# Optimization experiments

Measured on AMD Instinct MI355X. Metric: run time of the kernel, lower is better.

The kernel has to match this reference:

```python
import jax, jax.numpy as jnp
import numpy as np

N_NODES = 100000
N_EDGES = 800000
F_IN = 64
UNITS = 64


def setup_inputs() -> dict:
    key = jax.random.key(0)
    k1, k2, k3, k4, k5, k6 = jax.random.split(key, 6)
    x = jax.random.normal(k1, (N_NODES, F_IN), dtype=jnp.float32)
    w = jax.random.normal(k2, (F_IN, UNITS), dtype=jnp.float32)
    b = jax.random.normal(k3, (UNITS,), dtype=jnp.float32)
    edge_weight = jax.random.uniform(k4, (N_EDGES,), dtype=jnp.float32)
    edge_row = jax.random.randint(k5, (N_EDGES,), 0, N_NODES, dtype=jnp.int32)
    edge_col = jax.random.randint(k6, (N_EDGES,), 0, N_NODES, dtype=jnp.int32)
    return {"x": x, "w": w, "b": b, "edge_weight": edge_weight,
            "edge_row": edge_row, "edge_col": edge_col}


def reference(x, w, b, edge_weight, edge_row, edge_col):
    # GCN layer: out = A_hat @ (X W) + b, A_hat given in COO form.
    xw = jnp.matmul(x, w)                          # [N, units] dense projection
    msgs = xw[edge_col] * edge_weight[:, None]     # [E, units] gather + scale
    out = jax.ops.segment_sum(msgs, edge_row, num_segments=N_NODES)  # SpMM reduce
    return out + b
```

## Files before the change

### kernel.cpp

```cpp
#include <hip/hip_runtime.h>
#include <hip/hip_fp16.h>

#define N_NODES 100000
#define N_EDGES 800000
#define FDIM 64
#define TILE_ROWS 32
#define N_TILES (N_NODES / TILE_ROWS)
#define SCAN_BLOCK 1024
#define N_SCAN_BLOCKS ((N_NODES + SCAN_BLOCK - 1) / SCAN_BLOCK)

__global__ __launch_bounds__(256) void gemm_hist_kernel(
    const float* __restrict__ x, const float* __restrict__ w,
    const int* __restrict__ erow, __half* __restrict__ xwh,
    int* __restrict__ count) {
    const int tid = threadIdx.x;
    const int bid = blockIdx.x;

    const int e = bid * 256 + tid;
    if (e < N_EDGES) atomicAdd(&count[erow[e]], 1);

    __shared__ float wq[16 * 64 * 4];
    __shared__ float xs[TILE_ROWS * FDIM];

    const int lane = tid & 63;
    const int wid = tid >> 6;

    float4* wq4 = reinterpret_cast<float4*>(wq);
    #pragma unroll
    for (int it = 0; it < 4; ++it) {
        const int k0 = wid * 4 + it;
        float4 wv;
        wv.x = w[(4 * k0 + 0) * FDIM + lane];
        wv.y = w[(4 * k0 + 1) * FDIM + lane];
        wv.z = w[(4 * k0 + 2) * FDIM + lane];
        wv.w = w[(4 * k0 + 3) * FDIM + lane];
        wq4[k0 * 64 + lane] = wv;
    }

    {
        const float4* xg4 = reinterpret_cast<const float4*>(
            x + (size_t)bid * TILE_ROWS * FDIM);
        float4* xs4 = reinterpret_cast<float4*>(xs);
        xs4[tid] = xg4[tid];
        xs4[256 + tid] = xg4[256 + tid];
    }
    __syncthreads();

    const float4* xs4 = reinterpret_cast<const float4*>(xs);
    const int rbase = wid * 8;
    float acc[8] = {0.f, 0.f, 0.f, 0.f, 0.f, 0.f, 0.f, 0.f};
    #pragma unroll 4
    for (int k0 = 0; k0 < 16; ++k0) {
        const float4 wv = wq4[k0 * 64 + lane];
        #pragma unroll
        for (int rr = 0; rr < 8; ++rr) {
            const float4 xv = xs4[(rbase + rr) * 16 + k0];
            acc[rr] += xv.x * wv.x + xv.y * wv.y + xv.z * wv.z + xv.w * wv.w;
        }
    }

    const int growbase = bid * TILE_ROWS + rbase;
    #pragma unroll
    for (int rr = 0; rr < 8; ++rr)
        xwh[(size_t)(growbase + rr) * FDIM + lane] = __float2half(acc[rr]);
}

__global__ __launch_bounds__(SCAN_BLOCK) void scan_block_kernel(
    const int* __restrict__ count, int* __restrict__ starts,
    int* __restrict__ blockSums) {
    __shared__ int tmp[SCAN_BLOCK];
    const int tid = threadIdx.x;
    const int i = blockIdx.x * SCAN_BLOCK + tid;
    const int v = (i < N_NODES) ? count[i] : 0;
    tmp[tid] = v;
    __syncthreads();
    for (int off = 1; off < SCAN_BLOCK; off <<= 1) {
        int t = (tid >= off) ? tmp[tid - off] : 0;
        __syncthreads();
        tmp[tid] += t;
        __syncthreads();
    }
    if (i < N_NODES) starts[i] = tmp[tid] - v;
    if (tid == SCAN_BLOCK - 1) blockSums[blockIdx.x] = tmp[tid];
}

__global__ __launch_bounds__(256) void scanadd_kernel(
    int* __restrict__ starts, const int* __restrict__ blockSums,
    int* __restrict__ cursor) {
    __shared__ int ssum[128];
    const int tid = threadIdx.x;
    if (tid < 128) ssum[tid] = (tid < N_SCAN_BLOCKS) ? blockSums[tid] : 0;
    __syncthreads();
    for (int off = 1; off < 128; off <<= 1) {
        int t = (tid < 128 && tid >= off) ? ssum[tid - off] : 0;
        __syncthreads();
        if (tid < 128) ssum[tid] += t;
        __syncthreads();
    }
    const int i = blockIdx.x * 256 + tid;
    if (i < N_NODES) {
        const int j = i >> 10;
        const int add = (j == 0) ? 0 : ssum[j - 1];
        const int s = starts[i] + add;
        starts[i] = s;
        cursor[i] = s;
    } else if (i == N_NODES) {
        starts[N_NODES] = N_EDGES;
    }
}

__global__ __launch_bounds__(256) void fill_kernel(
    const int* __restrict__ erow, const int* __restrict__ ecol,
    const float* __restrict__ ew, int* __restrict__ cursor,
    uint2* __restrict__ recs) {
    const int base = (blockIdx.x * 256 + threadIdx.x) * 4;
    if (base + 3 < N_EDGES) {
        int4 r = *reinterpret_cast<const int4*>(erow + base);
        int4 c = *reinterpret_cast<const int4*>(ecol + base);
        float4 wt = *reinterpret_cast<const float4*>(ew + base);
        int p0 = atomicAdd(&cursor[r.x], 1);
        int p1 = atomicAdd(&cursor[r.y], 1);
        int p2 = atomicAdd(&cursor[r.z], 1);
        int p3 = atomicAdd(&cursor[r.w], 1);
        recs[p0] = make_uint2((unsigned)c.x, __float_as_uint(wt.x));
        recs[p1] = make_uint2((unsigned)c.y, __float_as_uint(wt.y));
        recs[p2] = make_uint2((unsigned)c.z, __float_as_uint(wt.z));
        recs[p3] = make_uint2((unsigned)c.w, __float_as_uint(wt.w));
    } else {
        for (int e = base; e < N_EDGES; ++e) {
            int p = atomicAdd(&cursor[erow[e]], 1);
            recs[p] = make_uint2((unsigned)ecol[e], __float_as_uint(ew[e]));
        }
    }
}

__global__ __launch_bounds__(256) void aggregate_h_kernel(
    const __half* __restrict__ xwh, const uint2* __restrict__ recs,
    const int* __restrict__ starts, const float* __restrict__ b,
    float* __restrict__ out) {
    const int lane = threadIdx.x & 63;
    const int g = lane >> 4;
    const int s = lane & 15;
    const int wave = (int)((blockIdx.x * blockDim.x + threadIdx.x) >> 6);
    const int nwaves = (int)((gridDim.x * (size_t)blockDim.x) >> 6);
    const float4 bias = reinterpret_cast<const float4*>(b)[s];
    const unsigned long long* recs8 =
        reinterpret_cast<const unsigned long long*>(recs);

    for (int r0 = wave * 4; r0 < N_NODES; r0 += nwaves * 4) {
        const int r = r0 + g;
        if (r < N_NODES) {
            const int st = starts[r];
            const int cnt = starts[r + 1] - st;
            float4 acc = bias;
            int k = 0;
            for (; k + 4 <= cnt; k += 4) {
                unsigned long long p0 = __builtin_nontemporal_load(recs8 + st + k + 0);
                unsigned long long p1 = __builtin_nontemporal_load(recs8 + st + k + 1);
                unsigned long long p2 = __builtin_nontemporal_load(recs8 + st + k + 2);
                unsigned long long p3 = __builtin_nontemporal_load(recs8 + st + k + 3);
                uint2 g0 = *reinterpret_cast<const uint2*>(
                    xwh + (size_t)(unsigned)p0 * FDIM + 4 * s);
                uint2 g1 = *reinterpret_cast<const uint2*>(
                    xwh + (size_t)(unsigned)p1 * FDIM + 4 * s);
                uint2 g2 = *reinterpret_cast<const uint2*>(
                    xwh + (size_t)(unsigned)p2 * FDIM + 4 * s);
                uint2 g3 = *reinterpret_cast<const uint2*>(
                    xwh + (size_t)(unsigned)p3 * FDIM + 4 * s);
                const float w0 = __uint_as_float((unsigned)(p0 >> 32));
                const float w1 = __uint_as_float((unsigned)(p1 >> 32));
                const float w2 = __uint_as_float((unsigned)(p2 >> 32));
                const float w3 = __uint_as_float((unsigned)(p3 >> 32));
                float2 a0 = __half22float2(*reinterpret_cast<__half2*>(&g0.x));
                float2 b0 = __half22float2(*reinterpret_cast<__half2*>(&g0.y));
                float2 a1 = __half22float2(*reinterpret_cast<__half2*>(&g1.x));
                float2 b1 = __half22float2(*reinterpret_cast<__half2*>(&g1.y));
                float2 a2 = __half22float2(*reinterpret_cast<__half2*>(&g2.x));
                float2 b2 = __half22float2(*reinterpret_cast<__half2*>(&g2.y));
                float2 a3 = __half22float2(*reinterpret_cast<__half2*>(&g3.x));
                float2 b3 = __half22float2(*reinterpret_cast<__half2*>(&g3.y));
                acc.x += a0.x * w0 + a1.x * w1 + a2.x * w2 + a3.x * w3;
                acc.y += a0.y * w0 + a1.y * w1 + a2.y * w2 + a3.y * w3;
                acc.z += b0.x * w0 + b1.x * w1 + b2.x * w2 + b3.x * w3;
                acc.w += b0.y * w0 + b1.y * w1 + b2.y * w2 + b3.y * w3;
            }
            for (; k < cnt; ++k) {
                unsigned long long p0 = __builtin_nontemporal_load(recs8 + st + k);
                uint2 g0 = *reinterpret_cast<const uint2*>(
                    xwh + (size_t)(unsigned)p0 * FDIM + 4 * s);
                const float w0 = __uint_as_float((unsigned)(p0 >> 32));
                float2 a0 = __half22float2(*reinterpret_cast<__half2*>(&g0.x));
                float2 b0 = __half22float2(*reinterpret_cast<__half2*>(&g0.y));
                acc.x += a0.x * w0; acc.y += a0.y * w0;
                acc.z += b0.x * w0; acc.w += b0.y * w0;
            }
            reinterpret_cast<float4*>(out + (size_t)r * FDIM)[s] = acc;
        }
    }
}

__global__ __launch_bounds__(256) void gemm_rm_kernel(
    const float* __restrict__ x, const float* __restrict__ w,
    float* __restrict__ xw) {
    const int lane = threadIdx.x & 63;
    float wr[FDIM];
    #pragma unroll
    for (int k = 0; k < FDIM; ++k) wr[k] = w[k * FDIM + lane];
    const int gwave = blockIdx.x * 4 + (threadIdx.x >> 6);
    const int nwaves = gridDim.x * 4;
    for (int row = gwave; row < N_NODES; row += nwaves) {
        const float4* xr = reinterpret_cast<const float4*>(x + (size_t)row * FDIM);
        float a0 = 0.f, a1 = 0.f, a2 = 0.f, a3 = 0.f;
        #pragma unroll
        for (int k0 = 0; k0 < FDIM / 4; ++k0) {
            float4 xv = xr[k0];
            a0 += xv.x * wr[4 * k0 + 0];
            a1 += xv.y * wr[4 * k0 + 1];
            a2 += xv.z * wr[4 * k0 + 2];
            a3 += xv.w * wr[4 * k0 + 3];
        }
        xw[(size_t)row * FDIM + lane] = (a0 + a1) + (a2 + a3);
    }
}

__global__ __launch_bounds__(256) void init_out_kernel(
    float* __restrict__ out, const float* __restrict__ b) {
    const float4* b4 = reinterpret_cast<const float4*>(b);
    float4* out4 = reinterpret_cast<float4*>(out);
    const size_t total = (size_t)N_NODES * FDIM / 4;
    size_t i = (size_t)blockIdx.x * blockDim.x + threadIdx.x;
    const size_t stride = (size_t)gridDim.x * blockDim.x;
    for (; i < total; i += stride) out4[i] = b4[i & 15];
}

__global__ __launch_bounds__(256) void scatter_kernel(
    const float* __restrict__ xw, const float* __restrict__ ew,
    const int* __restrict__ erow, const int* __restrict__ ecol,
    float* __restrict__ out) {
    const int lane = threadIdx.x & 63;
    const int g = lane >> 4;
    const int s = lane & 15;
    const int wave = (int)((blockIdx.x * blockDim.x + threadIdx.x) >> 6);
    const int nwaves = (int)((gridDim.x * (size_t)blockDim.x) >> 6);
    for (int e0 = wave * 4; e0 < N_EDGES; e0 += nwaves * 4) {
        const int e = e0 + g;
        if (e < N_EDGES) {
            const int c = ecol[e];
            const int r = erow[e];
            const float wgt = ew[e];
            const float4 v =
                reinterpret_cast<const float4*>(xw + (size_t)c * FDIM)[s];
            float* dst = out + (size_t)r * FDIM + 4 * s;
            atomicAdd(dst + 0, v.x * wgt);
            atomicAdd(dst + 1, v.y * wgt);
            atomicAdd(dst + 2, v.z * wgt);
            atomicAdd(dst + 3, v.w * wgt);
        }
    }
}

extern "C" void kernel_launch(void* const* d_in, const int* in_sizes, int n_in,
                              void* d_out, int out_size, void* d_ws, size_t ws_size,
                              hipStream_t stream) {
    const float* x  = (const float*)d_in[0];
    const float* w  = (const float*)d_in[1];
    const float* b  = (const float*)d_in[2];
    const float* ew = (const float*)d_in[3];
    const int* erow = (const int*)d_in[4];
    const int* ecol = (const int*)d_in[5];
    float* out = (float*)d_out;

    char* ws = (char*)d_ws;
    const size_t XWH_BYTES  = (size_t)N_NODES * FDIM * 2;
    const size_t REC_BYTES  = (size_t)N_EDGES * 8;
    const size_t CNT_BYTES  = (size_t)N_NODES * 4;
    const size_t ST_BYTES   = ((size_t)(N_NODES + 1) * 4 + 15) & ~(size_t)15;
    const size_t SUMS_BYTES = 512;
    const size_t NEED = XWH_BYTES + REC_BYTES + CNT_BYTES + ST_BYTES +
                        CNT_BYTES + SUMS_BYTES;

    if (ws_size >= NEED) {
        __half* xwh    = (__half*)ws;
        uint2* recs    = (uint2*)(ws + XWH_BYTES);
        int* count     = (int*)(ws + XWH_BYTES + REC_BYTES);
        int* starts    = (int*)(ws + XWH_BYTES + REC_BYTES + CNT_BYTES);
        int* cursor    = (int*)(ws + XWH_BYTES + REC_BYTES + CNT_BYTES + ST_BYTES);
        int* blockSums = (int*)(ws + XWH_BYTES + REC_BYTES + CNT_BYTES + ST_BYTES + CNT_BYTES);

        const int gE4 = (N_EDGES / 4 + 255) / 256;
        const int gN  = (N_NODES + 255) / 256 + 1;

        hipMemsetAsync(count, 0, CNT_BYTES, stream);
        gemm_hist_kernel<<<N_TILES, 256, 0, stream>>>(x, w, erow, xwh, count);
        scan_block_kernel<<<N_SCAN_BLOCKS, SCAN_BLOCK, 0, stream>>>(count, starts, blockSums);
        scanadd_kernel<<<gN, 256, 0, stream>>>(starts, blockSums, cursor);
        fill_kernel<<<gE4, 256, 0, stream>>>(erow, ecol, ew, cursor, recs);
        aggregate_h_kernel<<<2048, 256, 0, stream>>>(xwh, recs, starts, b, out);
    } else {
        float* xw = (float*)ws;
        gemm_rm_kernel<<<2048, 256, 0, stream>>>(x, w, xw);
        init_out_kernel<<<2048, 256, 0, stream>>>(out, b);
        scatter_kernel<<<2048, 256, 0, stream>>>(xw, ew, erow, ecol, out);
    }
}
```

Before: 203.8 us.

## Partition CSR fill atomics by XCD so each die owns a row subset

The fill kernel now launches eight times as many blocks. Each block handles only the edges whose row index matches its XCD slot (blockIdx & 7), so the atomics on a given cursor entry and the matching record writes come from a single die's L2. This is meant to cut cross-XCD atomic contention and coherence traffic. In exchange every edge chunk is read eight times, using nontemporal loads, and the number of wavefronts launched grows.

After: 197.7 us. -3.0%, faster.

```diff
diff --git a/kernel.cpp b/kernel.cpp
--- a/kernel.cpp
+++ b/kernel.cpp
@@ -8,6 +8,9 @@
 #define N_TILES (N_NODES / TILE_ROWS)
 #define SCAN_BLOCK 1024
 #define N_SCAN_BLOCKS ((N_NODES + SCAN_BLOCK - 1) / SCAN_BLOCK)
+
+typedef int   iv4 __attribute__((ext_vector_type(4)));
+typedef float fv4 __attribute__((ext_vector_type(4)));
 
 __global__ __launch_bounds__(256) void gemm_hist_kernel(
     const float* __restrict__ x, const float* __restrict__ w,
@@ -109,27 +112,35 @@
     }
 }
 
-__global__ __launch_bounds__(256) void fill_kernel(
+__global__ __launch_bounds__(256) void fill_xcd_kernel(
     const int* __restrict__ erow, const int* __restrict__ ecol,
     const float* __restrict__ ew, int* __restrict__ cursor,
     uint2* __restrict__ recs) {
-    const int base = (blockIdx.x * 256 + threadIdx.x) * 4;
+    const int xcd = blockIdx.x & 7;
+    const int chunk = blockIdx.x >> 3;
+    const int base = (chunk * 256 + threadIdx.x) * 4;
     if (base + 3 < N_EDGES) {
-        int4 r = *reinterpret_cast<const int4*>(erow + base);
-        int4 c = *reinterpret_cast<const int4*>(ecol + base);
-        float4 wt = *reinterpret_cast<const float4*>(ew + base);
-        int p0 = atomicAdd(&cursor[r.x], 1);
-        int p1 = atomicAdd(&cursor[r.y], 1);
-        int p2 = atomicAdd(&cursor[r.z], 1);
-        int p3 = atomicAdd(&cursor[r.w], 1);
-        recs[p0] = make_uint2((unsigned)c.x, __float_as_uint(wt.x));
-        recs[p1] = make_uint2((unsigned)c.y, __float_as_uint(wt.y));
-        recs[p2] = make_uint2((unsigned)c.z, __float_as_uint(wt.z));
-        recs[p3] = make_uint2((unsigned)c.w, __float_as_uint(wt.w));
+        iv4 r = __builtin_nontemporal_load(
+            reinterpret_cast<const iv4*>(erow + base));
+        iv4 c = __builtin_nontemporal_load(
+            reinterpret_cast<const iv4*>(ecol + base));
+        fv4 wt = __builtin_nontemporal_load(
+            reinterpret_cast<const fv4*>(ew + base));
+        #pragma unroll
+        for (int j = 0; j < 4; ++j) {
+            const int rr = r[j];
+            if ((rr & 7) == xcd) {
+                const int p = atomicAdd(&cursor[rr], 1);
+                recs[p] = make_uint2((unsigned)c[j], __float_as_uint(wt[j]));
+            }
+        }
     } else {
         for (int e = base; e < N_EDGES; ++e) {
-            int p = atomicAdd(&cursor[erow[e]], 1);
-            recs[p] = make_uint2((unsigned)ecol[e], __float_as_uint(ew[e]));
+            const int rr = erow[e];
+            if ((rr & 7) == xcd) {
+                const int p = atomicAdd(&cursor[rr], 1);
+                recs[p] = make_uint2((unsigned)ecol[e], __float_as_uint(ew[e]));
+            }
         }
     }
 }
@@ -294,7 +305,7 @@
         gemm_hist_kernel<<<N_TILES, 256, 0, stream>>>(x, w, erow, xwh, count);
         scan_block_kernel<<<N_SCAN_BLOCKS, SCAN_BLOCK, 0, stream>>>(count, starts, blockSums);
         scanadd_kernel<<<gN, 256, 0, stream>>>(starts, blockSums, cursor);
-        fill_kernel<<<gE4, 256, 0, stream>>>(erow, ecol, ew, cursor, recs);
+        fill_xcd_kernel<<<gE4 * 8, 256, 0, stream>>>(erow, ecol, ew, cursor, recs);
         aggregate_h_kernel<<<2048, 256, 0, stream>>>(xwh, recs, starts, b, out);
     } else {
         float* xw = (float*)ws;
```
